# Optimization experiments

Hardware: AMD Instinct MI355X
Metric: run time of the kernel (lower is better)

Reference implementation:

```python
import jax, jax.numpy as jnp
import numpy as np

B, F, R, O = 32768, 64, 64, 64  # batch, in_features, rules, out_features


def setup_inputs() -> dict:
    key = jax.random.key(0)
    k1, k2, k3, k4, k5 = jax.random.split(key, 5)
    X = jax.random.normal(k1, (B, F), dtype=jnp.float32)
    tt = jax.random.normal(k2, (1, F, R), dtype=jnp.float32) * 0.01
    mean = jax.random.normal(k3, (1, F, R), dtype=jnp.float32)
    # std is a learned positive scale (set by _rule_initialization); keep it away from 0
    std = jax.random.uniform(k4, (1, F, R), dtype=jnp.float32, minval=0.5, maxval=1.5)
    W = jax.random.normal(k5, (O, R * (F + 1)), dtype=jnp.float32) * 0.02  # nn.Linear weight [out, in]
    return {"X": X, "tt": tt, "mean": mean, "std": std, "W": W}


def reference(X, tt, mean, std, W):
    t = jnp.tanh(tt)                                  # [1,F,R]
    z = (X[:, :, None] - mean) / std                  # [B,F,R]
    g = jnp.exp(-(z * z))                             # Gaussian membership [B,F,R]
    m = g * t + 0.5 * (1.0 - t)                       # affine blend toward 0.5
    fire = jnp.prod(m, axis=1)                        # product t-norm over features -> [B,R]
    w = fire / jnp.sum(fire, axis=1, keepdims=True)   # normalize over rules
    ones = jnp.ones((X.shape[0], 1), dtype=X.dtype)
    Xa = jnp.concatenate([X, ones], axis=1)           # [B,F+1]
    feat = (Xa[:, :, None] * w[:, None, :]).reshape(X.shape[0], -1)  # [B,(F+1)*R], row-major (f outer, r inner)
    return feat @ W.T                                 # [B,O]
```

## Files before the change

kernel.cpp:

```cpp
#include <hip/hip_runtime.h>
#include <hip/hip_bf16.h>

#define F 64
#define R 64
#define O 64
#define BLOCK_B 32

typedef short bf16x8 __attribute__((ext_vector_type(8)));
typedef float f32x4 __attribute__((ext_vector_type(4)));
typedef float f32x2 __attribute__((ext_vector_type(2)));

static __device__ __forceinline__ unsigned short f2bf(float f) {
    unsigned u = __builtin_bit_cast(unsigned, f);
    unsigned r = (u + 0x7fffu + ((u >> 16) & 1u)) >> 16;
    return (unsigned short)r;
}

__global__ __launch_bounds__(256) void fq_prep(
        const float* __restrict__ tt, const float* __restrict__ mean,
        const float* __restrict__ std_, const float* __restrict__ W,
        float* __restrict__ prm, unsigned short* __restrict__ Wpk)
{
    const int tg = blockIdx.x * 256 + threadIdx.x;
    if (tg < 65 * 512) {
        const int f    = tg >> 9;
        const int u8   = tg & 511;
        const int lane = u8 & 63;
        const int kk   = (u8 >> 6) & 1;
        const int nt   = u8 >> 7;
        const int o    = nt * 16 + (lane & 15);
        const int rb   = ((lane >> 4) << 3) + kk * 32;
        const float* src = W + o * 4160 + f * 64 + rb;
        unsigned short v[8];
#pragma unroll
        for (int j = 0; j < 8; ++j) v[j] = f2bf(src[j]);
        const int dst = ((nt * 65 + f) * 2 + kk) * 64 + lane;
        *(bf16x8*)(Wpk + (size_t)dst * 8) = *(bf16x8*)v;
    } else if (tg < 65 * 512 + 4096) {
        const int u = tg - 65 * 512;
        float sd = std_[u];
        float mn = mean[u];
        float th = tanhf(tt[u]);
        float s  = 1.2011224087864498f / sd;
        float4 p;
        p.x = s;
        p.y = mn * s;
        p.z = th;
        p.w = 0.5f * (1.0f - th);
        ((float4*)prm)[u] = p;
    }
}

__global__ __launch_bounds__(256, 4) void fq_main(
        const float* __restrict__ X,
        const float4* __restrict__ prm,
        const bf16x8* __restrict__ Wp,
        float* __restrict__ out)
{
    __shared__ __align__(16) float xt[64][36];
    __shared__ __align__(16) unsigned short fireb[32][72];
    __shared__ __align__(16) float rinv[BLOCK_B];

    const int t    = threadIdx.x;
    const int lane = t & 63;
    const int w    = __builtin_amdgcn_readfirstlane(t >> 6);
    const int b0   = blockIdx.x * BLOCK_B;
    const int nt   = w;

    const int xrow = t >> 3;
    const int xf8  = (t & 7) * 8;
    float4 xh0 = *(const float4*)(X + (size_t)(b0 + xrow) * 64 + xf8);
    float4 xh1 = *(const float4*)(X + (size_t)(b0 + xrow) * 64 + xf8 + 4);

    const bf16x8* wpb = Wp + (size_t)(nt * 130) * 64 + lane;
    bf16x8 pe0 = wpb[0 * 64],  pe1 = wpb[1 * 64];
    bf16x8 po0 = wpb[2 * 64],  po1 = wpb[3 * 64];

    {
        f32x2 fire2[4];
#pragma unroll
        for (int i = 0; i < 4; ++i) fire2[i] = (f32x2){1.f, 1.f};
        const float* Xw = X + (size_t)(b0 + 8 * w) * 64;
        float4 p = prm[lane];
#pragma unroll 2
        for (int f = 0; f < F; ++f) {
            const int pf = (f + 1 < 64) ? f + 1 : 63;
            float4 pn = prm[pf * 64 + lane];
            f32x2 px = (f32x2){p.x, p.x};
            f32x2 py = (f32x2){-p.y, -p.y};
            f32x2 pt = (f32x2){p.z, p.z};
            f32x2 pc = (f32x2){p.w, p.w};
#pragma unroll
            for (int i = 0; i < 4; ++i) {
                f32x2 x;
                x.x = Xw[(2 * i) * 64 + f];
                x.y = Xw[(2 * i + 1) * 64 + f];
                f32x2 z  = __builtin_elementwise_fma(x, px, py);
                f32x2 nz = -(z * z);
                f32x2 g;
                g.x = __builtin_amdgcn_exp2f(nz.x);
                g.y = __builtin_amdgcn_exp2f(nz.y);
                f32x2 m = __builtin_elementwise_fma(g, pt, pc);
                fire2[i] = fire2[i] * m;
            }
            p = pn;
        }
#pragma unroll
        for (int j = 0; j < 4; ++j) {
            xt[xf8 + j][xrow]     = xh0[j];
            xt[xf8 + 4 + j][xrow] = xh1[j];
        }
        const int r0 = 8 * w;
#pragma unroll
        for (int i = 0; i < 4; ++i) {
            fireb[r0 + 2 * i][lane]     = f2bf(fire2[i].x);
            fireb[r0 + 2 * i + 1][lane] = f2bf(fire2[i].y);
        }
#pragma unroll
        for (int i = 0; i < 4; ++i) {
            float sx = fire2[i].x, sy = fire2[i].y;
#pragma unroll
            for (int d = 1; d < 64; d <<= 1) {
                sx += __shfl_xor(sx, d);
                sy += __shfl_xor(sy, d);
            }
            if (lane == 0) {
                rinv[r0 + 2 * i]     = 1.0f / sx;
                rinv[r0 + 2 * i + 1] = 1.0f / sy;
            }
        }
    }
    __syncthreads();

    const int m_in = lane & 15;
    const int quad = lane >> 4;
    const int q16  = quad * 16;

    bf16x8 wfrag[2][2];
#pragma unroll
    for (int mm = 0; mm < 2; ++mm) {
        const int myrow = 16 * mm + m_in;
        wfrag[mm][0] = *(const bf16x8*)((const char*)&fireb[myrow][0] + q16);
        wfrag[mm][1] = *(const bf16x8*)((const char*)&fireb[myrow][32] + q16);
    }

    f32x4 acc[2];
    acc[0] = (f32x4){0.f, 0.f, 0.f, 0.f};
    acc[1] = (f32x4){0.f, 0.f, 0.f, 0.f};
    const f32x4 z4 = (f32x4){0.f, 0.f, 0.f, 0.f};

#pragma unroll 2
    for (int i = 0; i < 32; ++i) {
        const int fe = 2 * i, fo = 2 * i + 1;
        bf16x8 ce0 = pe0, ce1 = pe1, co0 = po0, co1 = po1;
        const int se = (fe + 2 <= 64) ? fe + 2 : 64;
        const int so = (fo + 2 <= 64) ? fo + 2 : 64;
        pe0 = wpb[(2 * se) * 64];  pe1 = wpb[(2 * se + 1) * 64];
        po0 = wpb[(2 * so) * 64];  po1 = wpb[(2 * so + 1) * 64];
#pragma unroll
        for (int mm = 0; mm < 2; ++mm) {
            f32x4 U = __builtin_amdgcn_mfma_f32_16x16x32_bf16(wfrag[mm][0], ce0, z4, 0, 0, 0);
            U = __builtin_amdgcn_mfma_f32_16x16x32_bf16(wfrag[mm][1], ce1, U, 0, 0, 0);
            f32x4 xv = *(const f32x4*)&xt[fe][16 * mm + quad * 4];
#pragma unroll
            for (int reg = 0; reg < 4; ++reg)
                acc[mm][reg] = __builtin_fmaf(xv[reg], U[reg], acc[mm][reg]);
        }
#pragma unroll
        for (int mm = 0; mm < 2; ++mm) {
            f32x4 U = __builtin_amdgcn_mfma_f32_16x16x32_bf16(wfrag[mm][0], co0, z4, 0, 0, 0);
            U = __builtin_amdgcn_mfma_f32_16x16x32_bf16(wfrag[mm][1], co1, U, 0, 0, 0);
            f32x4 xv = *(const f32x4*)&xt[fo][16 * mm + quad * 4];
#pragma unroll
            for (int reg = 0; reg < 4; ++reg)
                acc[mm][reg] = __builtin_fmaf(xv[reg], U[reg], acc[mm][reg]);
        }
    }

#pragma unroll
    for (int mm = 0; mm < 2; ++mm) {
        f32x4 U = __builtin_amdgcn_mfma_f32_16x16x32_bf16(wfrag[mm][0], pe0, z4, 0, 0, 0);
        U = __builtin_amdgcn_mfma_f32_16x16x32_bf16(wfrag[mm][1], pe1, U, 0, 0, 0);
#pragma unroll
        for (int reg = 0; reg < 4; ++reg)
            acc[mm][reg] += U[reg];
    }

#pragma unroll
    for (int mm = 0; mm < 2; ++mm) {
        f32x4 rv = *(const f32x4*)&rinv[16 * mm + quad * 4];
#pragma unroll
        for (int reg = 0; reg < 4; ++reg) {
            const int row = b0 + 16 * mm + quad * 4 + reg;
            out[(size_t)row * 64 + nt * 16 + m_in] = acc[mm][reg] * rv[reg];
        }
    }
}

extern "C" void kernel_launch(void* const* d_in, const int* in_sizes, int n_in,
                              void* d_out, int out_size, void* d_ws, size_t ws_size,
                              hipStream_t stream) {
    const float* X    = (const float*)d_in[0];
    const float* tt   = (const float*)d_in[1];
    const float* mean = (const float*)d_in[2];
    const float* std_ = (const float*)d_in[3];
    const float* W    = (const float*)d_in[4];
    float* out = (float*)d_out;

    float* prm = (float*)d_ws;
    unsigned short* Wpk = (unsigned short*)((char*)d_ws + 65536);

    fq_prep<<<146, 256, 0, stream>>>(tt, mean, std_, W, prm, Wpk);

    const int nblocks = 32768 / BLOCK_B;
    fq_main<<<nblocks, 256, 0, stream>>>(X, (const float4*)prm,
                                         (const bf16x8*)Wpk, out);
}
```

Measured before the change: 104.3 us.

## Process two 32-row tiles per block, overlapping second tile's membership with first tile's MFMA

Each block now handles 64 batch rows as two 32-row tiles with double-buffered shared memory. The exp-heavy membership/firing computation of the second tile is interleaved into the MFMA contraction loop of the first tile, so VALU transcendental work and matrix work can overlap within a wave. The grid halves to 512 blocks, which reduces parallelism and raises register pressure in the fused loop.

```diff
diff --git a/kernel.cpp b/kernel.cpp
--- a/kernel.cpp
+++ b/kernel.cpp
@@ -4,7 +4,6 @@
 #define F 64
 #define R 64
 #define O 64
-#define BLOCK_B 32
 
 typedef short bf16x8 __attribute__((ext_vector_type(8)));
 typedef float f32x4 __attribute__((ext_vector_type(4)));
@@ -57,22 +56,27 @@
         const bf16x8* __restrict__ Wp,
         float* __restrict__ out)
 {
-    __shared__ __align__(16) float xt[64][36];
-    __shared__ __align__(16) unsigned short fireb[32][72];
-    __shared__ __align__(16) float rinv[BLOCK_B];
+    __shared__ __align__(16) float xt[2][64][36];
+    __shared__ __align__(16) unsigned short fireb[2][32][72];
+    __shared__ __align__(16) float rinv[2][32];
 
     const int t    = threadIdx.x;
     const int lane = t & 63;
     const int w    = __builtin_amdgcn_readfirstlane(t >> 6);
-    const int b0   = blockIdx.x * BLOCK_B;
     const int nt   = w;
-
+    const int b0   = blockIdx.x * 64;
+
+    const int m_in = lane & 15;
+    const int quad = lane >> 4;
+    const int q16  = quad * 16;
     const int xrow = t >> 3;
     const int xf8  = (t & 7) * 8;
-    float4 xh0 = *(const float4*)(X + (size_t)(b0 + xrow) * 64 + xf8);
-    float4 xh1 = *(const float4*)(X + (size_t)(b0 + xrow) * 64 + xf8 + 4);
 
     const bf16x8* wpb = Wp + (size_t)(nt * 130) * 64 + lane;
+    const f32x4 z4 = (f32x4){0.f, 0.f, 0.f, 0.f};
+
+    float4 xa0 = *(const float4*)(X + (size_t)(b0 + xrow) * 64 + xf8);
+    float4 xa1 = *(const float4*)(X + (size_t)(b0 + xrow) * 64 + xf8 + 4);
     bf16x8 pe0 = wpb[0 * 64],  pe1 = wpb[1 * 64];
     bf16x8 po0 = wpb[2 * 64],  po1 = wpb[3 * 64];
 
@@ -107,14 +111,14 @@
         }
 #pragma unroll
         for (int j = 0; j < 4; ++j) {
-            xt[xf8 + j][xrow]     = xh0[j];
-            xt[xf8 + 4 + j][xrow] = xh1[j];
+            xt[0][xf8 + j][xrow]     = xa0[j];
+            xt[0][xf8 + 4 + j][xrow] = xa1[j];
         }
         const int r0 = 8 * w;
 #pragma unroll
         for (int i = 0; i < 4; ++i) {
-            fireb[r0 + 2 * i][lane]     = f2bf(fire2[i].x);
-            fireb[r0 + 2 * i + 1][lane] = f2bf(fire2[i].y);
+            fireb[0][r0 + 2 * i][lane]     = f2bf(fire2[i].x);
+            fireb[0][r0 + 2 * i + 1][lane] = f2bf(fire2[i].y);
         }
 #pragma unroll
         for (int i = 0; i < 4; ++i) {
@@ -125,74 +129,208 @@
                 sy += __shfl_xor(sy, d);
             }
             if (lane == 0) {
-                rinv[r0 + 2 * i]     = 1.0f / sx;
-                rinv[r0 + 2 * i + 1] = 1.0f / sy;
+                rinv[0][r0 + 2 * i]     = 1.0f / sx;
+                rinv[0][r0 + 2 * i + 1] = 1.0f / sy;
             }
         }
     }
     __syncthreads();
 
-    const int m_in = lane & 15;
-    const int quad = lane >> 4;
-    const int q16  = quad * 16;
-
-    bf16x8 wfrag[2][2];
-#pragma unroll
-    for (int mm = 0; mm < 2; ++mm) {
-        const int myrow = 16 * mm + m_in;
-        wfrag[mm][0] = *(const bf16x8*)((const char*)&fireb[myrow][0] + q16);
-        wfrag[mm][1] = *(const bf16x8*)((const char*)&fireb[myrow][32] + q16);
+    {
+        bf16x8 wfrag[2][2];
+#pragma unroll
+        for (int mm = 0; mm < 2; ++mm) {
+            const int myrow = 16 * mm + m_in;
+            wfrag[mm][0] = *(const bf16x8*)((const char*)&fireb[0][myrow][0] + q16);
+            wfrag[mm][1] = *(const bf16x8*)((const char*)&fireb[0][myrow][32] + q16);
+        }
+        f32x4 acc[2];
+        acc[0] = z4; acc[1] = z4;
+
+        float4 xb0 = *(const float4*)(X + (size_t)(b0 + 32 + xrow) * 64 + xf8);
+        float4 xb1 = *(const float4*)(X + (size_t)(b0 + 32 + xrow) * 64 + xf8 + 4);
+        f32x2 fire2[4];
+#pragma unroll
+        for (int i = 0; i < 4; ++i) fire2[i] = (f32x2){1.f, 1.f};
+        const float* Xw = X + (size_t)(b0 + 32 + 8 * w) * 64;
+        float4 p = prm[lane];
+
+#pragma unroll 1
+        for (int i = 0; i < 32; ++i) {
+            const int fe = 2 * i, fo = 2 * i + 1;
+            bf16x8 ce0 = pe0, ce1 = pe1, co0 = po0, co1 = po1;
+            const int se = (fe + 2 <= 64) ? fe + 2 : 64;
+            const int so = (fo + 2 <= 64) ? fo + 2 : 64;
+            pe0 = wpb[(2 * se) * 64];  pe1 = wpb[(2 * se + 1) * 64];
+            po0 = wpb[(2 * so) * 64];  po1 = wpb[(2 * so + 1) * 64];
+            float4 pn0 = prm[fo * 64 + lane];
+            const int pf1 = (fo + 1 < 64) ? fo + 1 : 63;
+            float4 pn1 = prm[pf1 * 64 + lane];
+
+#pragma unroll
+            for (int mm = 0; mm < 2; ++mm) {
+                f32x4 U = __builtin_amdgcn_mfma_f32_16x16x32_bf16(wfrag[mm][0], ce0, z4, 0, 0, 0);
+                U = __builtin_amdgcn_mfma_f32_16x16x32_bf16(wfrag[mm][1], ce1, U, 0, 0, 0);
+                f32x4 xv = *(const f32x4*)&xt[0][fe][16 * mm + quad * 4];
+#pragma unroll
+                for (int reg = 0; reg < 4; ++reg)
+                    acc[mm][reg] = __builtin_fmaf(xv[reg], U[reg], acc[mm][reg]);
+            }
+            {
+                f32x2 px = (f32x2){p.x, p.x};
+                f32x2 py = (f32x2){-p.y, -p.y};
+                f32x2 pt = (f32x2){p.z, p.z};
+                f32x2 pc = (f32x2){p.w, p.w};
+#pragma unroll
+                for (int i2 = 0; i2 < 4; ++i2) {
+                    f32x2 x;
+                    x.x = Xw[(2 * i2) * 64 + fe];
+                    x.y = Xw[(2 * i2 + 1) * 64 + fe];
+                    f32x2 z  = __builtin_elementwise_fma(x, px, py);
+                    f32x2 nz = -(z * z);
+                    f32x2 g;
+                    g.x = __builtin_amdgcn_exp2f(nz.x);
+                    g.y = __builtin_amdgcn_exp2f(nz.y);
+                    f32x2 m = __builtin_elementwise_fma(g, pt, pc);
+                    fire2[i2] = fire2[i2] * m;
+                }
+            }
+#pragma unroll
+            for (int mm = 0; mm < 2; ++mm) {
+                f32x4 U = __builtin_amdgcn_mfma_f32_16x16x32_bf16(wfrag[mm][0], co0, z4, 0, 0, 0);
+                U = __builtin_amdgcn_mfma_f32_16x16x32_bf16(wfrag[mm][1], co1, U, 0, 0, 0);
+                f32x4 xv = *(const f32x4*)&xt[0][fo][16 * mm + quad * 4];
+#pragma unroll
+                for (int reg = 0; reg < 4; ++reg)
+                    acc[mm][reg] = __builtin_fmaf(xv[reg], U[reg], acc[mm][reg]);
+            }
+            {
+                f32x2 px = (f32x2){pn0.x, pn0.x};
+                f32x2 py = (f32x2){-pn0.y, -pn0.y};
+                f32x2 pt = (f32x2){pn0.z, pn0.z};
+                f32x2 pc = (f32x2){pn0.w, pn0.w};
+#pragma unroll
+                for (int i2 = 0; i2 < 4; ++i2) {
+                    f32x2 x;
+                    x.x = Xw[(2 * i2) * 64 + fo];
+                    x.y = Xw[(2 * i2 + 1) * 64 + fo];
+                    f32x2 z  = __builtin_elementwise_fma(x, px, py);
+                    f32x2 nz = -(z * z);
+                    f32x2 g;
+                    g.x = __builtin_amdgcn_exp2f(nz.x);
+                    g.y = __builtin_amdgcn_exp2f(nz.y);
+                    f32x2 m = __builtin_elementwise_fma(g, pt, pc);
+                    fire2[i2] = fire2[i2] * m;
+                }
+            }
+            p = pn1;
+        }
+
+#pragma unroll
+        for (int mm = 0; mm < 2; ++mm) {
+            f32x4 U = __builtin_amdgcn_mfma_f32_16x16x32_bf16(wfrag[mm][0], pe0, z4, 0, 0, 0);
+            U = __builtin_amdgcn_mfma_f32_16x16x32_bf16(wfrag[mm][1], pe1, U, 0, 0, 0);
+#pragma unroll
+            for (int reg = 0; reg < 4; ++reg)
+                acc[mm][reg] += U[reg];
+        }
+
+        pe0 = wpb[0 * 64];  pe1 = wpb[1 * 64];
+        po0 = wpb[2 * 64];  po1 = wpb[3 * 64];
+
+#pragma unroll
+        for (int mm = 0; mm < 2; ++mm) {
+            f32x4 rv = *(const f32x4*)&rinv[0][16 * mm + quad * 4];
+#pragma unroll
+            for (int reg = 0; reg < 4; ++reg) {
+                const int row = b0 + 16 * mm + quad * 4 + reg;
+                out[(size_t)row * 64 + nt * 16 + m_in] = acc[mm][reg] * rv[reg];
+            }
+        }
+
+#pragma unroll
+        for (int j = 0; j < 4; ++j) {
+            xt[1][xf8 + j][xrow]     = xb0[j];
+            xt[1][xf8 + 4 + j][xrow] = xb1[j];
+        }
+        const int r0 = 8 * w;
+#pragma unroll
+        for (int i = 0; i < 4; ++i) {
+            fireb[1][r0 + 2 * i][lane]     = f2bf(fire2[i].x);
+            fireb[1][r0 + 2 * i + 1][lane] = f2bf(fire2[i].y);
+        }
+#pragma unroll
+        for (int i = 0; i < 4; ++i) {
+            float sx = fire2[i].x, sy = fire2[i].y;
+#pragma unroll
+            for (int d = 1; d < 64; d <<= 1) {
+                sx += __shfl_xor(sx, d);
+                sy += __shfl_xor(sy, d);
+            }
+            if (lane == 0) {
+                rinv[1][r0 + 2 * i]     = 1.0f / sx;
+                rinv[1][r0 + 2 * i + 1] = 1.0f / sy;
+            }
+        }
     }
-
-    f32x4 acc[2];
-    acc[0] = (f32x4){0.f, 0.f, 0.f, 0.f};
-    acc[1] = (f32x4){0.f, 0.f, 0.f, 0.f};
-    const f32x4 z4 = (f32x4){0.f, 0.f, 0.f, 0.f};
+    __syncthreads();
+
+    {
+        bf16x8 wfrag[2][2];
+#pragma unroll
+        for (int mm = 0; mm < 2; ++mm) {
+            const int myrow = 16 * mm + m_in;
+            wfrag[mm][0] = *(const bf16x8*)((const char*)&fireb[1][myrow][0] + q16);
+            wfrag[mm][1] = *(const bf16x8*)((const char*)&fireb[1][myrow][32] + q16);
+        }
+        f32x4 acc[2];
+        acc[0] = z4; acc[1] = z4;
 
 #pragma unroll 2
-    for (int i = 0; i < 32; ++i) {
-        const int fe = 2 * i, fo = 2 * i + 1;
-        bf16x8 ce0 = pe0, ce1 = pe1, co0 = po0, co1 = po1;
-        const int se = (fe + 2 <= 64) ? fe + 2 : 64;
-        const int so = (fo + 2 <= 64) ? fo + 2 : 64;
-        pe0 = wpb[(2 * se) * 64];  pe1 = wpb[(2 * se + 1) * 64];
-        po0 = wpb[(2 * so) * 64];  po1 = wpb[(2 * so + 1) * 64];
-#pragma unroll
-        for (int mm = 0; mm < 2; ++mm) {
-            f32x4 U = __builtin_amdgcn_mfma_f32_16x16x32_bf16(wfrag[mm][0], ce0, z4, 0, 0, 0);
-            U = __builtin_amdgcn_mfma_f32_16x16x32_bf16(wfrag[mm][1], ce1, U, 0, 0, 0);
-            f32x4 xv = *(const f32x4*)&xt[fe][16 * mm + quad * 4];
+        for (int i = 0; i < 32; ++i) {
+            const int fe = 2 * i, fo = 2 * i + 1;
+            bf16x8 ce0 = pe0, ce1 = pe1, co0 = po0, co1 = po1;
+            const int se = (fe + 2 <= 64) ? fe + 2 : 64;
+            const int so = (fo + 2 <= 64) ? fo + 2 : 64;
+            pe0 = wpb[(2 * se) * 64];  pe1 = wpb[(2 * se + 1) * 64];
+            po0 = wpb[(2 * so) * 64];  po1 = wpb[(2 * so + 1) * 64];
+#pragma unroll
+            for (int mm = 0; mm < 2; ++mm) {
+                f32x4 U = __builtin_amdgcn_mfma_f32_16x16x32_bf16(wfrag[mm][0], ce0, z4, 0, 0, 0);
+                U = __builtin_amdgcn_mfma_f32_16x16x32_bf16(wfrag[mm][1], ce1, U, 0, 0, 0);
+                f32x4 xv = *(const f32x4*)&xt[1][fe][16 * mm + quad * 4];
+#pragma unroll
+                for (int reg = 0; reg < 4; ++reg)
+                    acc[mm][reg] = __builtin_fmaf(xv[reg], U[reg], acc[mm][reg]);
+            }
+#pragma unroll
+            for (int mm = 0; mm < 2; ++mm) {
+                f32x4 U = __builtin_amdgcn_mfma_f32_16x16x32_bf16(wfrag[mm][0], co0, z4, 0, 0, 0);
+                U = __builtin_amdgcn_mfma_f32_16x16x32_bf16(wfrag[mm][1], co1, U, 0, 0, 0);
+                f32x4 xv = *(const f32x4*)&xt[1][fo][16 * mm + quad * 4];
+#pragma unroll
+                for (int reg = 0; reg < 4; ++reg)
+                    acc[mm][reg] = __builtin_fmaf(xv[reg], U[reg], acc[mm][reg]);
+            }
+        }
+
+#pragma unroll
+        for (int mm = 0; mm < 2; ++mm) {
+            f32x4 U = __builtin_amdgcn_mfma_f32_16x16x32_bf16(wfrag[mm][0], pe0, z4, 0, 0, 0);
+            U = __builtin_amdgcn_mfma_f32_16x16x32_bf16(wfrag[mm][1], pe1, U, 0, 0, 0);
 #pragma unroll
             for (int reg = 0; reg < 4; ++reg)
-                acc[mm][reg] = __builtin_fmaf(xv[reg], U[reg], acc[mm][reg]);
-        }
-#pragma unroll
-        for (int mm = 0; mm < 2; ++mm) {
-            f32x4 U = __builtin_amdgcn_mfma_f32_16x16x32_bf16(wfrag[mm][0], co0, z4, 0, 0, 0);
-            U = __builtin_amdgcn_mfma_f32_16x16x32_bf16(wfrag[mm][1], co1, U, 0, 0, 0);
-            f32x4 xv = *(const f32x4*)&xt[fo][16 * mm + quad * 4];
-#pragma unroll
-            for (int reg = 0; reg < 4; ++reg)
-                acc[mm][reg] = __builtin_fmaf(xv[reg], U[reg], acc[mm][reg]);
-        }
-    }
-
-#pragma unroll
-    for (int mm = 0; mm < 2; ++mm) {
-        f32x4 U = __builtin_amdgcn_mfma_f32_16x16x32_bf16(wfrag[mm][0], pe0, z4, 0, 0, 0);
-        U = __builtin_amdgcn_mfma_f32_16x16x32_bf16(wfrag[mm][1], pe1, U, 0, 0, 0);
-#pragma unroll
-        for (int reg = 0; reg < 4; ++reg)
-            acc[mm][reg] += U[reg];
-    }
-
-#pragma unroll
-    for (int mm = 0; mm < 2; ++mm) {
-        f32x4 rv = *(const f32x4*)&rinv[16 * mm + quad * 4];
-#pragma unroll
-        for (int reg = 0; reg < 4; ++reg) {
-            const int row = b0 + 16 * mm + quad * 4 + reg;
-            out[(size_t)row * 64 + nt * 16 + m_in] = acc[mm][reg] * rv[reg];
+                acc[mm][reg] += U[reg];
+        }
+
+#pragma unroll
+        for (int mm = 0; mm < 2; ++mm) {
+            f32x4 rv = *(const f32x4*)&rinv[1][16 * mm + quad * 4];
+#pragma unroll
+            for (int reg = 0; reg < 4; ++reg) {
+                const int row = b0 + 32 + 16 * mm + quad * 4 + reg;
+                out[(size_t)row * 64 + nt * 16 + m_in] = acc[mm][reg] * rv[reg];
+            }
         }
     }
 }
@@ -212,7 +350,7 @@
 
     fq_prep<<<146, 256, 0, stream>>>(tt, mean, std_, W, prm, Wpk);
 
-    const int nblocks = 32768 / BLOCK_B;
+    const int nblocks = 512;
     fq_main<<<nblocks, 256, 0, stream>>>(X, (const float4*)prm,
                                          (const bf16x8*)Wpk, out);
 }
```

Result: slower. 108.2 us (+3.7%).

## Split fused kernel into separate firing-strength and GEMM kernels

Applied to the files above, without the earlier changes.

Splits the fused kernel into two. One kernel computes per-row rule firing strengths and their reciprocal sums into workspace, using fewer rows per wave for higher occupancy. A second kernel runs the MFMA GEMM over 128-row tiles with 1024-thread blocks. This decouples the exp-heavy stage from the matrix stage at the cost of a global memory round-trip for the bf16 firing matrix and an extra launch.

```diff
diff --git a/kernel.cpp b/kernel.cpp
--- a/kernel.cpp
+++ b/kernel.cpp
@@ -4,7 +4,6 @@
 #define F 64
 #define R 64
 #define O 64
-#define BLOCK_B 32
 
 typedef short bf16x8 __attribute__((ext_vector_type(8)));
 typedef float f32x4 __attribute__((ext_vector_type(4)));
@@ -51,103 +50,114 @@
     }
 }
 
-__global__ __launch_bounds__(256, 4) void fq_main(
+__global__ __launch_bounds__(256, 8) void fq_fire(
         const float* __restrict__ X,
         const float4* __restrict__ prm,
+        unsigned short* __restrict__ fireb,
+        float* __restrict__ rinvg)
+{
+    const int t    = threadIdx.x;
+    const int lane = t & 63;
+    const int w    = __builtin_amdgcn_readfirstlane(t >> 6);
+    const int row0 = (blockIdx.x * 4 + w) * 4;
+
+    f32x2 fire2[2] = {(f32x2){1.f, 1.f}, (f32x2){1.f, 1.f}};
+    const float* Xw = X + (size_t)row0 * 64;
+    float4 p = prm[lane];
+#pragma unroll 4
+    for (int f = 0; f < F; ++f) {
+        const int pf = (f + 1 < 64) ? f + 1 : 63;
+        float4 pn = prm[pf * 64 + lane];
+        f32x2 px = (f32x2){p.x, p.x};
+        f32x2 py = (f32x2){-p.y, -p.y};
+        f32x2 pt = (f32x2){p.z, p.z};
+        f32x2 pc = (f32x2){p.w, p.w};
+#pragma unroll
+        for (int i = 0; i < 2; ++i) {
+            f32x2 x;
+            x.x = Xw[(2 * i) * 64 + f];
+            x.y = Xw[(2 * i + 1) * 64 + f];
+            f32x2 z  = __builtin_elementwise_fma(x, px, py);
+            f32x2 nz = -(z * z);
+            f32x2 g;
+            g.x = __builtin_amdgcn_exp2f(nz.x);
+            g.y = __builtin_amdgcn_exp2f(nz.y);
+            f32x2 m = __builtin_elementwise_fma(g, pt, pc);
+            fire2[i] = fire2[i] * m;
+        }
+        p = pn;
+    }
+
+#pragma unroll
+    for (int i = 0; i < 2; ++i) {
+        fireb[(size_t)(row0 + 2 * i) * 64 + lane]     = f2bf(fire2[i].x);
+        fireb[(size_t)(row0 + 2 * i + 1) * 64 + lane] = f2bf(fire2[i].y);
+    }
+#pragma unroll
+    for (int i = 0; i < 2; ++i) {
+        float sx = fire2[i].x, sy = fire2[i].y;
+#pragma unroll
+        for (int d = 1; d < 64; d <<= 1) {
+            sx += __shfl_xor(sx, d);
+            sy += __shfl_xor(sy, d);
+        }
+        if (lane == 0) {
+            rinvg[row0 + 2 * i]     = 1.0f / sx;
+            rinvg[row0 + 2 * i + 1] = 1.0f / sy;
+        }
+    }
+}
+
+__global__ __launch_bounds__(1024, 4) void fq_gemm(
+        const float* __restrict__ X,
+        const unsigned short* __restrict__ fireb,
+        const float* __restrict__ rinvg,
         const bf16x8* __restrict__ Wp,
         float* __restrict__ out)
 {
-    __shared__ __align__(16) float xt[64][36];
-    __shared__ __align__(16) unsigned short fireb[32][72];
-    __shared__ __align__(16) float rinv[BLOCK_B];
+    __shared__ __align__(16) float xt[64][132];
 
     const int t    = threadIdx.x;
     const int lane = t & 63;
     const int w    = __builtin_amdgcn_readfirstlane(t >> 6);
-    const int b0   = blockIdx.x * BLOCK_B;
-    const int nt   = w;
-
-    const int xrow = t >> 3;
-    const int xf8  = (t & 7) * 8;
-    float4 xh0 = *(const float4*)(X + (size_t)(b0 + xrow) * 64 + xf8);
-    float4 xh1 = *(const float4*)(X + (size_t)(b0 + xrow) * 64 + xf8 + 4);
+    const int nt   = w >> 2;
+    const int g    = w & 3;
+    const int b0   = blockIdx.x * 128;
+
+    const int m_in = lane & 15;
+    const int quad = lane >> 4;
+    const int q8   = quad * 8;
+    const f32x4 z4 = (f32x4){0.f, 0.f, 0.f, 0.f};
 
     const bf16x8* wpb = Wp + (size_t)(nt * 130) * 64 + lane;
     bf16x8 pe0 = wpb[0 * 64],  pe1 = wpb[1 * 64];
     bf16x8 po0 = wpb[2 * 64],  po1 = wpb[3 * 64];
 
+    bf16x8 wfrag[2][2];
+    f32x4 rv[2];
+#pragma unroll
+    for (int mm = 0; mm < 2; ++mm) {
+        const int myrow = b0 + 32 * g + 16 * mm + m_in;
+        wfrag[mm][0] = *(const bf16x8*)(fireb + (size_t)myrow * 64 + q8);
+        wfrag[mm][1] = *(const bf16x8*)(fireb + (size_t)myrow * 64 + q8 + 32);
+        rv[mm] = *(const f32x4*)(rinvg + b0 + 32 * g + 16 * mm + quad * 4);
+    }
+
     {
-        f32x2 fire2[4];
-#pragma unroll
-        for (int i = 0; i < 4; ++i) fire2[i] = (f32x2){1.f, 1.f};
-        const float* Xw = X + (size_t)(b0 + 8 * w) * 64;
-        float4 p = prm[lane];
-#pragma unroll 2
-        for (int f = 0; f < F; ++f) {
-            const int pf = (f + 1 < 64) ? f + 1 : 63;
-            float4 pn = prm[pf * 64 + lane];
-            f32x2 px = (f32x2){p.x, p.x};
-            f32x2 py = (f32x2){-p.y, -p.y};
-            f32x2 pt = (f32x2){p.z, p.z};
-            f32x2 pc = (f32x2){p.w, p.w};
-#pragma unroll
-            for (int i = 0; i < 4; ++i) {
-                f32x2 x;
-                x.x = Xw[(2 * i) * 64 + f];
-                x.y = Xw[(2 * i + 1) * 64 + f];
-                f32x2 z  = __builtin_elementwise_fma(x, px, py);
-                f32x2 nz = -(z * z);
-                f32x2 g;
-                g.x = __builtin_amdgcn_exp2f(nz.x);
-                g.y = __builtin_amdgcn_exp2f(nz.y);
-                f32x2 m = __builtin_elementwise_fma(g, pt, pc);
-                fire2[i] = fire2[i] * m;
-            }
-            p = pn;
-        }
+        const int xrow = t >> 3;
+        const int xf8  = (t & 7) * 8;
+        float4 x0 = *(const float4*)(X + (size_t)(b0 + xrow) * 64 + xf8);
+        float4 x1 = *(const float4*)(X + (size_t)(b0 + xrow) * 64 + xf8 + 4);
 #pragma unroll
         for (int j = 0; j < 4; ++j) {
-            xt[xf8 + j][xrow]     = xh0[j];
-            xt[xf8 + 4 + j][xrow] = xh1[j];
-        }
-        const int r0 = 8 * w;
-#pragma unroll
-        for (int i = 0; i < 4; ++i) {
-            fireb[r0 + 2 * i][lane]     = f2bf(fire2[i].x);
-            fireb[r0 + 2 * i + 1][lane] = f2bf(fire2[i].y);
-        }
-#pragma unroll
-        for (int i = 0; i < 4; ++i) {
-            float sx = fire2[i].x, sy = fire2[i].y;
-#pragma unroll
-            for (int d = 1; d < 64; d <<= 1) {
-                sx += __shfl_xor(sx, d);
-                sy += __shfl_xor(sy, d);
-            }
-            if (lane == 0) {
-                rinv[r0 + 2 * i]     = 1.0f / sx;
-                rinv[r0 + 2 * i + 1] = 1.0f / sy;
-            }
+            xt[xf8 + j][xrow]     = x0[j];
+            xt[xf8 + 4 + j][xrow] = x1[j];
         }
     }
     __syncthreads();
 
-    const int m_in = lane & 15;
-    const int quad = lane >> 4;
-    const int q16  = quad * 16;
-
-    bf16x8 wfrag[2][2];
-#pragma unroll
-    for (int mm = 0; mm < 2; ++mm) {
-        const int myrow = 16 * mm + m_in;
-        wfrag[mm][0] = *(const bf16x8*)((const char*)&fireb[myrow][0] + q16);
-        wfrag[mm][1] = *(const bf16x8*)((const char*)&fireb[myrow][32] + q16);
-    }
-
     f32x4 acc[2];
-    acc[0] = (f32x4){0.f, 0.f, 0.f, 0.f};
-    acc[1] = (f32x4){0.f, 0.f, 0.f, 0.f};
-    const f32x4 z4 = (f32x4){0.f, 0.f, 0.f, 0.f};
+    acc[0] = z4; acc[1] = z4;
 
 #pragma unroll 2
     for (int i = 0; i < 32; ++i) {
@@ -161,7 +171,7 @@
         for (int mm = 0; mm < 2; ++mm) {
             f32x4 U = __builtin_amdgcn_mfma_f32_16x16x32_bf16(wfrag[mm][0], ce0, z4, 0, 0, 0);
             U = __builtin_amdgcn_mfma_f32_16x16x32_bf16(wfrag[mm][1], ce1, U, 0, 0, 0);
-            f32x4 xv = *(const f32x4*)&xt[fe][16 * mm + quad * 4];
+            f32x4 xv = *(const f32x4*)&xt[fe][32 * g + 16 * mm + quad * 4];
 #pragma unroll
             for (int reg = 0; reg < 4; ++reg)
                 acc[mm][reg] = __builtin_fmaf(xv[reg], U[reg], acc[mm][reg]);
@@ -170,7 +180,7 @@
         for (int mm = 0; mm < 2; ++mm) {
             f32x4 U = __builtin_amdgcn_mfma_f32_16x16x32_bf16(wfrag[mm][0], co0, z4, 0, 0, 0);
             U = __builtin_amdgcn_mfma_f32_16x16x32_bf16(wfrag[mm][1], co1, U, 0, 0, 0);
-            f32x4 xv = *(const f32x4*)&xt[fo][16 * mm + quad * 4];
+            f32x4 xv = *(const f32x4*)&xt[fo][32 * g + 16 * mm + quad * 4];
 #pragma unroll
             for (int reg = 0; reg < 4; ++reg)
                 acc[mm][reg] = __builtin_fmaf(xv[reg], U[reg], acc[mm][reg]);
@@ -187,14 +197,12 @@
     }
 
 #pragma unroll
-    for (int mm = 0; mm < 2; ++mm) {
-        f32x4 rv = *(const f32x4*)&rinv[16 * mm + quad * 4];
+    for (int mm = 0; mm < 2; ++mm)
 #pragma unroll
         for (int reg = 0; reg < 4; ++reg) {
-            const int row = b0 + 16 * mm + quad * 4 + reg;
-            out[(size_t)row * 64 + nt * 16 + m_in] = acc[mm][reg] * rv[reg];
-        }
-    }
+            const int row = b0 + 32 * g + 16 * mm + quad * 4 + reg;
+            out[(size_t)row * 64 + nt * 16 + m_in] = acc[mm][reg] * rv[mm][reg];
+        }
 }
 
 extern "C" void kernel_launch(void* const* d_in, const int* in_sizes, int n_in,
@@ -207,12 +215,12 @@
     const float* W    = (const float*)d_in[4];
     float* out = (float*)d_out;
 
-    float* prm = (float*)d_ws;
-    unsigned short* Wpk = (unsigned short*)((char*)d_ws + 65536);
+    float* prm           = (float*)d_ws;
+    unsigned short* Wpk  = (unsigned short*)((char*)d_ws + 65536);
+    unsigned short* fb   = (unsigned short*)((char*)d_ws + 655360);
+    float* rinvg         = (float*)((char*)d_ws + 4849664);
 
     fq_prep<<<146, 256, 0, stream>>>(tt, mean, std_, W, prm, Wpk);
-
-    const int nblocks = 32768 / BLOCK_B;
-    fq_main<<<nblocks, 256, 0, stream>>>(X, (const float4*)prm,
-                                         (const bf16x8*)Wpk, out);
-}
+    fq_fire<<<2048, 256, 0, stream>>>(X, (const float4*)prm, fb, rinvg);
+    fq_gemm<<<256, 1024, 0, stream>>>(X, fb, rinvg, (const bf16x8*)Wpk, out);
+}
```

New measurement: 112.3 us. 7.7% more time.
